# Kernel optimization log

Measured on AMD Instinct MI355X. Metric: run time of the kernel, lower is better.

The kernel has to match this reference:

```python
import jax, jax.numpy as jnp
import numpy as np

D_MODEL = 1024
NUM_HEADS = 16
HEAD_DIM = D_MODEL // NUM_HEADS


def setup_inputs() -> dict:
    key = jax.random.key(0)
    ks = jax.random.split(key, 9)
    s = 1.0 / np.sqrt(D_MODEL)
    x = jax.random.normal(ks[0], (2, 2048, D_MODEL), dtype=jnp.float32)
    Wq = jax.random.normal(ks[1], (D_MODEL, D_MODEL), dtype=jnp.float32) * s
    bq = jnp.zeros((D_MODEL,), dtype=jnp.float32)
    Wk = jax.random.normal(ks[2], (D_MODEL, D_MODEL), dtype=jnp.float32) * s
    bk = jnp.zeros((D_MODEL,), dtype=jnp.float32)
    Wv = jax.random.normal(ks[3], (D_MODEL, D_MODEL), dtype=jnp.float32) * s
    bv = jnp.zeros((D_MODEL,), dtype=jnp.float32)
    Wo = jax.random.normal(ks[4], (D_MODEL, D_MODEL), dtype=jnp.float32) * s
    bo = jnp.zeros((D_MODEL,), dtype=jnp.float32)
    return {"x": x, "Wq": Wq, "bq": bq, "Wk": Wk, "bk": bk,
            "Wv": Wv, "bv": bv, "Wo": Wo, "bo": bo}


def reference(x, Wq, bq, Wk, bk, Wv, bv, Wo, bo):
    B, S, D = x.shape
    H, Hd = NUM_HEADS, HEAD_DIM
    scale = 1.0 / np.sqrt(Hd)

    def split_heads(t):  # [B,S,D] -> [B,H,S,Hd]
        return t.reshape(B, S, H, Hd).transpose(0, 2, 1, 3)

    q = split_heads(x @ Wq + bq)
    k = split_heads(x @ Wk + bk)
    v = split_heads(x @ Wv + bv)

    scores = jnp.einsum('bhqd,bhkd->bhqk', q, k) * scale
    scores = scores - jnp.max(scores, axis=-1, keepdims=True)
    attn = jax.nn.softmax(scores, axis=-1)
    attended = jnp.einsum('bhqk,bhkd->bhqd', attn, v)
    attended = attended.transpose(0, 2, 1, 3).reshape(B, S, D)
    return attended @ Wo + bo
```

## Files before the change

kernel.cpp:

```cpp
#include <hip/hip_runtime.h>
#include <hip/hip_bf16.h>

typedef __bf16 bf16_t;
typedef __bf16 bf16x8 __attribute__((ext_vector_type(8)));
typedef __bf16 bf16x4 __attribute__((ext_vector_type(4)));
typedef float floatx4 __attribute__((ext_vector_type(4)));
typedef short short4v __attribute__((ext_vector_type(4)));

#define D_MODEL 1024
#define SEQ     2048
#define BATCH   2
#define NHEAD   16
#define HDIM    64
#define MTOT    (BATCH * SEQ)

#define QSCALE  0.18033688011112042f

union PBu { bf16x4 b; short4v s; };

__device__ __forceinline__ void async_copy16(const bf16_t* g, bf16_t* l) {
    __builtin_amdgcn_global_load_lds(
        (const __attribute__((address_space(1))) void*)g,
        (__attribute__((address_space(3))) void*)l, 16, 0, 0);
}

__global__ void cvt_f32_bf16(const float* __restrict__ x, bf16_t* __restrict__ y, int n) {
    int i = (blockIdx.x * 256 + threadIdx.x) * 4;
    if (i < n) {
        const float4 v = *(const float4*)(x + i);
        bf16x4 o = { (bf16_t)v.x, (bf16_t)v.y, (bf16_t)v.z, (bf16_t)v.w };
        *(bf16x4*)(y + i) = o;
    }
}

__global__ void transpose_w4(
    const float* __restrict__ W0, const float* __restrict__ W1,
    const float* __restrict__ W2, const float* __restrict__ W3,
    bf16_t* __restrict__ T0, bf16_t* __restrict__ T1,
    bf16_t* __restrict__ T2, bf16_t* __restrict__ T3)
{
    __shared__ float tile[32][33];
    const int z = blockIdx.z;
    const float* W = (z == 0) ? W0 : (z == 1) ? W1 : (z == 2) ? W2 : W3;
    bf16_t*     Wt = (z == 0) ? T0 : (z == 1) ? T1 : (z == 2) ? T2 : T3;
    const int tx = threadIdx.x, ty = threadIdx.y;
    const int k0 = blockIdx.y * 32, n0 = blockIdx.x * 32;
#pragma unroll
    for (int j = 0; j < 32; j += 8)
        tile[ty + j][tx] = W[(size_t)(k0 + ty + j) * D_MODEL + n0 + tx];
    __syncthreads();
#pragma unroll
    for (int j = 0; j < 32; j += 8)
        Wt[(size_t)(n0 + ty + j) * D_MODEL + k0 + tx] = (bf16_t)tile[tx][ty + j];
}

__device__ __forceinline__ void gemm_mainloop(
    const bf16_t* __restrict__ A, const bf16_t* __restrict__ Bt,
    int m0, int n0, bf16_t* As, bf16_t* Bs, floatx4 acc[4][4])
{
    const int tid  = threadIdx.x;
    const int lane = tid & 63;
    const int wid  = tid >> 6;
    const int quad = lane >> 4;
    const int col  = lane & 15;
    const int wm   = (wid >> 1) * 64;
    const int wn   = (wid & 1) * 64;
    const int srow = tid >> 3;
    const int scc  = ((tid & 7) ^ (srow & 7)) * 8;
    const int xorc = col & 7;

    const bf16_t* Ag = A  + (size_t)(m0 + srow) * D_MODEL + scc;
    const bf16_t* Bg = Bt + (size_t)(n0 + srow) * D_MODEL + scc;
    bf16_t* Al = As + tid * 8;
    bf16_t* Bl = Bs + tid * 8;

    for (int kb = 0; kb < D_MODEL; kb += 64) {
#pragma unroll
        for (int p = 0; p < 4; ++p) {
            async_copy16(Ag + kb + p * (32 * D_MODEL), Al + p * 2048);
            async_copy16(Bg + kb + p * (32 * D_MODEL), Bl + p * 2048);
        }
        __syncthreads();
#pragma unroll
        for (int kh = 0; kh < 2; ++kh) {
            bf16x8 af[4], bfr[4];
#pragma unroll
            for (int i = 0; i < 4; ++i)
                af[i] = *(const bf16x8*)(As + (wm + i * 16 + col) * 64 + (((kh * 4 + quad) ^ xorc) * 8));
#pragma unroll
            for (int j = 0; j < 4; ++j)
                bfr[j] = *(const bf16x8*)(Bs + (wn + j * 16 + col) * 64 + (((kh * 4 + quad) ^ xorc) * 8));
#pragma unroll
            for (int i = 0; i < 4; ++i)
#pragma unroll
                for (int j = 0; j < 4; ++j)
                    acc[i][j] = __builtin_amdgcn_mfma_f32_16x16x32_bf16(af[i], bfr[j], acc[i][j], 0, 0, 0);
        }
        __syncthreads();
    }
}

__global__ __launch_bounds__(256, 3) void gemm_qkv(
    const bf16_t* __restrict__ xb,
    const bf16_t* __restrict__ Wtq, const bf16_t* __restrict__ Wtk, const bf16_t* __restrict__ Wtv,
    const float* __restrict__ bq, const float* __restrict__ bk, const float* __restrict__ bv,
    bf16_t* __restrict__ Q, bf16_t* __restrict__ Kh, bf16_t* __restrict__ Vt)
{
    __shared__ bf16_t As[128 * 64];
    __shared__ bf16_t Bs[128 * 64];
    const int z = blockIdx.z;
    const bf16_t* Bt   = (z == 0) ? Wtq : (z == 1) ? Wtk : Wtv;
    const float*  bias = (z == 0) ? bq  : (z == 1) ? bk  : bv;
    bf16_t*       O    = (z == 0) ? Q   : (z == 1) ? Kh  : Vt;
    const float   qs   = (z == 0) ? QSCALE : 1.0f;
    const int m0 = blockIdx.y * 128;
    const int n0 = blockIdx.x * 128;

    floatx4 acc[4][4];
#pragma unroll
    for (int i = 0; i < 4; ++i)
#pragma unroll
        for (int j = 0; j < 4; ++j)
            acc[i][j] = (floatx4){0.f, 0.f, 0.f, 0.f};

    gemm_mainloop(xb, Bt, m0, n0, As, Bs, acc);

    const int tid  = threadIdx.x;
    const int lane = tid & 63;
    const int wid  = tid >> 6;
    const int quad = lane >> 4;
    const int col  = lane & 15;
    const int wm   = (wid >> 1) * 64;
    const int wn   = (wid & 1) * 64;

    if (z == 2) {
#pragma unroll
        for (int i = 0; i < 4; ++i) {
#pragma unroll
            for (int j = 0; j < 4; ++j) {
                const int n = n0 + wn + j * 16 + col;
                const float bb = bias[n];
                const int mb = m0 + wm + i * 16 + quad * 4;
                const size_t bhb = (size_t)((mb >> 11) * NHEAD + (n >> 6)) * (SEQ * HDIM);
                bf16x4 pk = { (bf16_t)(acc[i][j][0] + bb), (bf16_t)(acc[i][j][1] + bb),
                              (bf16_t)(acc[i][j][2] + bb), (bf16_t)(acc[i][j][3] + bb) };
                *(bf16x4*)(O + bhb + (size_t)(n & 63) * SEQ + (mb & 2047)) = pk;
            }
        }
    } else {
#pragma unroll
        for (int i = 0; i < 4; ++i) {
#pragma unroll
            for (int j = 0; j < 4; ++j) {
                const int n = n0 + wn + j * 16 + col;
                const float bb = bias[n];
#pragma unroll
                for (int r = 0; r < 4; ++r) {
                    const int m = m0 + wm + i * 16 + quad * 4 + r;
                    const float v = (acc[i][j][r] + bb) * qs;
                    const size_t bhb = (size_t)((m >> 11) * NHEAD + (n >> 6)) * (SEQ * HDIM);
                    O[bhb + (size_t)(m & 2047) * HDIM + (n & 63)] = (bf16_t)v;
                }
            }
        }
    }
}

__global__ __launch_bounds__(256, 2) void attn_kernel(
    const bf16_t* __restrict__ Q, const bf16_t* __restrict__ K,
    const bf16_t* __restrict__ Vt, bf16_t* __restrict__ A2)
{
    __shared__ union SM {
        struct { bf16_t Ks[2][64 * 64]; bf16_t Vs[2][64 * 64]; } t;
        struct { float Ored[2][64 * 68]; float Lred[2][64]; } r;
    } sm;

    const int tid  = threadIdx.x;
    const int lane = tid & 63;
    const int wid  = tid >> 6;
    const int quad = lane >> 4;
    const int col  = lane & 15;
    const int xorc = col & 7;
    const int qh   = wid & 1;
    const int kh   = wid >> 1;

    const int blk = blockIdx.x;
    const int idx = blk >> 3;
    const int bh  = (blk & 7) * 4 + (idx >> 4);
    const int q0  = (idx & 15) * 128;
    const int b   = bh >> 4, h = bh & 15;

    const bf16_t* Qb = Q  + (size_t)bh * (SEQ * HDIM);
    const bf16_t* Kb = K  + (size_t)bh * (SEQ * HDIM);
    const bf16_t* Vb = Vt + (size_t)bh * (SEQ * HDIM);

    bf16x8 qf[4][2];
#pragma unroll
    for (int g = 0; g < 4; ++g) {
        const int qrow = q0 + qh * 64 + g * 16 + col;
        qf[g][0] = *(const bf16x8*)(Qb + (size_t)qrow * HDIM + quad * 8);
        qf[g][1] = *(const bf16x8*)(Qb + (size_t)qrow * HDIM + 32 + quad * 8);
    }

    floatx4 o_acc[4][4];
    float lsum[4] = {0.f, 0.f, 0.f, 0.f};
#pragma unroll
    for (int g = 0; g < 4; ++g)
#pragma unroll
        for (int dt = 0; dt < 4; ++dt)
            o_acc[g][dt] = (floatx4){0.f, 0.f, 0.f, 0.f};

    const int srow = tid >> 3;
    const int scc  = ((tid & 7) ^ (srow & 7)) * 8;
    const bf16_t* Kg = Kb + (size_t)srow * HDIM + scc;
    const bf16_t* Vg = Vb + (size_t)srow * SEQ + scc;
    bf16_t* Ks0 = &sm.t.Ks[0][0];
    bf16_t* Ks1 = &sm.t.Ks[1][0];
    bf16_t* Vs0 = &sm.t.Vs[0][0];
    bf16_t* Vs1 = &sm.t.Vs[1][0];

    auto stage = [&](int ko, bf16_t* dk, bf16_t* dv) {
        async_copy16(Kg + (size_t)ko * HDIM, dk + tid * 8);
        async_copy16(Kg + (size_t)(ko + 32) * HDIM, dk + tid * 8 + 2048);
        async_copy16(Vg + ko, dv + tid * 8);
        async_copy16(Vg + (size_t)32 * SEQ + ko, dv + tid * 8 + 2048);
    };

    auto step = [&](const bf16_t* KsC, const bf16_t* VsC) {
        bf16x8 kf[2][2];
#pragma unroll
        for (int tt = 0; tt < 2; ++tt) {
            const int t = kh * 2 + tt;
            kf[tt][0] = *(const bf16x8*)(KsC + (t * 16 + col) * 64 + ((quad ^ xorc) * 8));
            kf[tt][1] = *(const bf16x8*)(KsC + (t * 16 + col) * 64 + (((4 + quad) ^ xorc) * 8));
        }
        short4v vfr[4][2];
#pragma unroll
        for (int dt = 0; dt < 4; ++dt)
#pragma unroll
            for (int tt = 0; tt < 2; ++tt) {
                const int t = kh * 2 + tt;
                const int sch = t * 2 + (quad >> 1);
                vfr[dt][tt] = *(const short4v*)(VsC + (dt * 16 + col) * 64 + ((sch ^ xorc) * 8) + (quad & 1) * 4);
            }
#pragma unroll
        for (int g = 0; g < 4; ++g) {
            floatx4 s_acc[2];
            short4v pb[2];
            __builtin_amdgcn_s_setprio(1);
#pragma unroll
            for (int tt = 0; tt < 2; ++tt) {
                s_acc[tt] = (floatx4){0.f, 0.f, 0.f, 0.f};
                s_acc[tt] = __builtin_amdgcn_mfma_f32_16x16x32_bf16(kf[tt][0], qf[g][0], s_acc[tt], 0, 0, 0);
                s_acc[tt] = __builtin_amdgcn_mfma_f32_16x16x32_bf16(kf[tt][1], qf[g][1], s_acc[tt], 0, 0, 0);
            }
            __builtin_amdgcn_s_setprio(0);
            float ls = 0.f;
#pragma unroll
            for (int tt = 0; tt < 2; ++tt) {
                const float p0 = __builtin_amdgcn_exp2f(s_acc[tt][0]);
                const float p1 = __builtin_amdgcn_exp2f(s_acc[tt][1]);
                const float p2 = __builtin_amdgcn_exp2f(s_acc[tt][2]);
                const float p3 = __builtin_amdgcn_exp2f(s_acc[tt][3]);
                ls += (p0 + p1) + (p2 + p3);
                PBu u;
                u.b = (bf16x4){ (bf16_t)p0, (bf16_t)p1, (bf16_t)p2, (bf16_t)p3 };
                pb[tt] = u.s;
            }
            lsum[g] += ls;
            __builtin_amdgcn_s_setprio(1);
#pragma unroll
            for (int dt = 0; dt < 4; ++dt)
#pragma unroll
                for (int tt = 0; tt < 2; ++tt)
                    o_acc[g][dt] = __builtin_amdgcn_mfma_f32_16x16x16bf16_1k(vfr[dt][tt], pb[tt], o_acc[g][dt], 0, 0, 0);
            __builtin_amdgcn_s_setprio(0);
        }
    };

    stage(0,  Ks0, Vs0);
    stage(64, Ks1, Vs1);

#pragma unroll 1
    for (int it2 = 0; it2 < 15; ++it2) {
        asm volatile("s_waitcnt vmcnt(4)" ::: "memory");
        __builtin_amdgcn_s_barrier();
        step(Ks0, Vs0);
        asm volatile("s_waitcnt lgkmcnt(0)" ::: "memory");
        __builtin_amdgcn_s_barrier();
        stage((2 * it2 + 2) * 64, Ks0, Vs0);

        asm volatile("s_waitcnt vmcnt(4)" ::: "memory");
        __builtin_amdgcn_s_barrier();
        step(Ks1, Vs1);
        asm volatile("s_waitcnt lgkmcnt(0)" ::: "memory");
        __builtin_amdgcn_s_barrier();
        stage((2 * it2 + 3) * 64, Ks1, Vs1);
    }
    asm volatile("s_waitcnt vmcnt(4)" ::: "memory");
    __builtin_amdgcn_s_barrier();
    step(Ks0, Vs0);
    asm volatile("s_waitcnt vmcnt(0)" ::: "memory");
    __builtin_amdgcn_s_barrier();
    step(Ks1, Vs1);

#pragma unroll
    for (int g = 0; g < 4; ++g) {
        lsum[g] += __shfl_xor(lsum[g], 16, 64);
        lsum[g] += __shfl_xor(lsum[g], 32, 64);
    }
    __syncthreads();
    if (kh == 1) {
#pragma unroll
        for (int g = 0; g < 4; ++g) {
#pragma unroll
            for (int dt = 0; dt < 4; ++dt)
#pragma unroll
                for (int r = 0; r < 4; ++r) {
                    const int d = dt * 16 + quad * 4 + r;
                    sm.r.Ored[qh][d * 68 + g * 16 + col] = o_acc[g][dt][r];
                }
            if (quad == 0)
                sm.r.Lred[qh][g * 16 + col] = lsum[g];
        }
    }
    __syncthreads();
    if (kh == 0) {
#pragma unroll
        for (int g = 0; g < 4; ++g) {
            const float l = lsum[g] + sm.r.Lred[qh][g * 16 + col];
            const float inv = 1.0f / l;
            const int qrow = q0 + qh * 64 + g * 16 + col;
            bf16_t* dst = A2 + ((size_t)(b * SEQ + qrow)) * D_MODEL + h * HDIM + quad * 4;
#pragma unroll
            for (int dt = 0; dt < 4; ++dt) {
                bf16x4 pk;
#pragma unroll
                for (int r = 0; r < 4; ++r) {
                    const int d = dt * 16 + quad * 4 + r;
                    pk[r] = (bf16_t)((o_acc[g][dt][r] + sm.r.Ored[qh][d * 68 + g * 16 + col]) * inv);
                }
                *(bf16x4*)(dst + dt * 16) = pk;
            }
        }
    }
}

__global__ __launch_bounds__(256, 3) void gemm_proj(
    const bf16_t* __restrict__ A2, const bf16_t* __restrict__ Wto,
    const float* __restrict__ bo, float* __restrict__ out)
{
    __shared__ bf16_t As[64 * 64];
    __shared__ bf16_t Bs[128 * 64];
    const int m0 = blockIdx.y * 64;
    const int n0 = blockIdx.x * 128;

    const int tid  = threadIdx.x;
    const int lane = tid & 63;
    const int wid  = tid >> 6;
    const int quad = lane >> 4;
    const int col  = lane & 15;
    const int wm   = (wid >> 1) * 32;
    const int wn   = (wid & 1) * 64;
    const int srow = tid >> 3;
    const int scc  = ((tid & 7) ^ (srow & 7)) * 8;
    const int xorc = col & 7;

    floatx4 acc[2][4];
#pragma unroll
    for (int i = 0; i < 2; ++i)
#pragma unroll
        for (int j = 0; j < 4; ++j)
            acc[i][j] = (floatx4){0.f, 0.f, 0.f, 0.f};

    const bf16_t* Ag = A2  + (size_t)(m0 + srow) * D_MODEL + scc;
    const bf16_t* Bg = Wto + (size_t)(n0 + srow) * D_MODEL + scc;
    bf16_t* Al = As + tid * 8;
    bf16_t* Bl = Bs + tid * 8;

    for (int kb = 0; kb < D_MODEL; kb += 64) {
#pragma unroll
        for (int p = 0; p < 2; ++p)
            async_copy16(Ag + kb + p * (32 * D_MODEL), Al + p * 2048);
#pragma unroll
        for (int p = 0; p < 4; ++p)
            async_copy16(Bg + kb + p * (32 * D_MODEL), Bl + p * 2048);
        __syncthreads();
#pragma unroll
        for (int kh = 0; kh < 2; ++kh) {
            bf16x8 af[2], bfr[4];
#pragma unroll
            for (int i = 0; i < 2; ++i)
                af[i] = *(const bf16x8*)(As + (wm + i * 16 + col) * 64 + (((kh * 4 + quad) ^ xorc) * 8));
#pragma unroll
            for (int j = 0; j < 4; ++j)
                bfr[j] = *(const bf16x8*)(Bs + (wn + j * 16 + col) * 64 + (((kh * 4 + quad) ^ xorc) * 8));
#pragma unroll
            for (int i = 0; i < 2; ++i)
#pragma unroll
                for (int j = 0; j < 4; ++j)
                    acc[i][j] = __builtin_amdgcn_mfma_f32_16x16x32_bf16(af[i], bfr[j], acc[i][j], 0, 0, 0);
        }
        __syncthreads();
    }

#pragma unroll
    for (int i = 0; i < 2; ++i) {
#pragma unroll
        for (int j = 0; j < 4; ++j) {
            const int n = n0 + wn + j * 16 + col;
            const float bb = bo[n];
#pragma unroll
            for (int r = 0; r < 4; ++r) {
                const int m = m0 + wm + i * 16 + quad * 4 + r;
                out[(size_t)m * D_MODEL + n] = acc[i][j][r] + bb;
            }
        }
    }
}

extern "C" void kernel_launch(void* const* d_in, const int* in_sizes, int n_in,
                              void* d_out, int out_size, void* d_ws, size_t ws_size,
                              hipStream_t stream) {
    const float* x  = (const float*)d_in[0];
    const float* Wq = (const float*)d_in[1];
    const float* bq = (const float*)d_in[2];
    const float* Wk = (const float*)d_in[3];
    const float* bk = (const float*)d_in[4];
    const float* Wv = (const float*)d_in[5];
    const float* bv = (const float*)d_in[6];
    const float* Wo = (const float*)d_in[7];
    const float* bo = (const float*)d_in[8];
    float* out = (float*)d_out;

    const size_t MB = 1ull << 20;
    char* ws = (char*)d_ws;
    bf16_t* Q     = (bf16_t*)(ws + 0 * MB);
    bf16_t* Kh    = (bf16_t*)(ws + 8 * MB);
    bf16_t* Vt    = (bf16_t*)(ws + 16 * MB);
    bf16_t* A2    = (bf16_t*)(ws + 24 * MB);
    bf16_t* xb    = (bf16_t*)(ws + 32 * MB);
    bf16_t* Wtq   = (bf16_t*)(ws + 40 * MB);
    bf16_t* Wtk   = (bf16_t*)(ws + 42 * MB);
    bf16_t* Wtv   = (bf16_t*)(ws + 44 * MB);
    bf16_t* Wto   = (bf16_t*)(ws + 46 * MB);

    const int nx = MTOT * D_MODEL;
    cvt_f32_bf16<<<nx / (256 * 4), 256, 0, stream>>>(x, xb, nx);

    transpose_w4<<<dim3(D_MODEL / 32, D_MODEL / 32, 4), dim3(32, 8), 0, stream>>>(
        Wq, Wk, Wv, Wo, Wtq, Wtk, Wtv, Wto);

    gemm_qkv<<<dim3(D_MODEL / 128, MTOT / 128, 3), 256, 0, stream>>>(
        xb, Wtq, Wtk, Wtv, bq, bk, bv, Q, Kh, Vt);

    attn_kernel<<<dim3(512), 256, 0, stream>>>(Q, Kh, Vt, A2);

    gemm_proj<<<dim3(D_MODEL / 128, MTOT / 64), 256, 0, stream>>>(A2, Wto, bo, out);
}
```

Measured before the change: 188.9 us.

## Software-pipeline PV MFMAs one tile behind QK and merge prep kernels

The attention inner loop now computes the QK scores and exponentials for the current K/V tile while issuing the P·V MFMAs for the previous tile. V fragments and P values are double-buffered in registers so exp/convert work can overlap matrix-core work. Separately, the x-to-bf16 conversion is folded into the weight-transpose kernel as an extra grid slice, which removes one launch. The added register buffers raise register pressure and may reduce occupancy.

```diff
diff --git a/kernel.cpp b/kernel.cpp
--- a/kernel.cpp
+++ b/kernel.cpp
@@ -24,16 +24,8 @@
         (__attribute__((address_space(3))) void*)l, 16, 0, 0);
 }
 
-__global__ void cvt_f32_bf16(const float* __restrict__ x, bf16_t* __restrict__ y, int n) {
-    int i = (blockIdx.x * 256 + threadIdx.x) * 4;
-    if (i < n) {
-        const float4 v = *(const float4*)(x + i);
-        bf16x4 o = { (bf16_t)v.x, (bf16_t)v.y, (bf16_t)v.z, (bf16_t)v.w };
-        *(bf16x4*)(y + i) = o;
-    }
-}
-
-__global__ void transpose_w4(
+__global__ void prep(
+    const float* __restrict__ x, bf16_t* __restrict__ xb,
     const float* __restrict__ W0, const float* __restrict__ W1,
     const float* __restrict__ W2, const float* __restrict__ W3,
     bf16_t* __restrict__ T0, bf16_t* __restrict__ T1,
@@ -41,9 +33,21 @@
 {
     __shared__ float tile[32][33];
     const int z = blockIdx.z;
+    const int tx = threadIdx.x, ty = threadIdx.y;
+    if (z == 4) {
+        const int tid = ty * 32 + tx;
+        const int base = (blockIdx.y * 32 + blockIdx.x) * 4096 + tid * 4;
+#pragma unroll
+        for (int r = 0; r < 4; ++r) {
+            const int i = base + r * 1024;
+            const float4 v = *(const float4*)(x + i);
+            bf16x4 o = { (bf16_t)v.x, (bf16_t)v.y, (bf16_t)v.z, (bf16_t)v.w };
+            *(bf16x4*)(xb + i) = o;
+        }
+        return;
+    }
     const float* W = (z == 0) ? W0 : (z == 1) ? W1 : (z == 2) ? W2 : W3;
     bf16_t*     Wt = (z == 0) ? T0 : (z == 1) ? T1 : (z == 2) ? T2 : T3;
-    const int tx = threadIdx.x, ty = threadIdx.y;
     const int k0 = blockIdx.y * 32, n0 = blockIdx.x * 32;
 #pragma unroll
     for (int j = 0; j < 32; j += 8)
@@ -226,7 +230,26 @@
         async_copy16(Vg + (size_t)32 * SEQ + ko, dv + tid * 8 + 2048);
     };
 
-    auto step = [&](const bf16_t* KsC, const bf16_t* VsC) {
+    short4v vfrA[4][2], vfrB[4][2];
+    short4v pbA[4][2],  pbB[4][2];
+
+    auto pv = [&](short4v (&vfrP)[4][2], short4v (&pbP)[4][2]) {
+        __builtin_amdgcn_s_setprio(1);
+#pragma unroll
+        for (int g = 0; g < 4; ++g)
+#pragma unroll
+            for (int dt = 0; dt < 4; ++dt)
+#pragma unroll
+                for (int tt = 0; tt < 2; ++tt)
+                    o_acc[g][dt] = __builtin_amdgcn_mfma_f32_16x16x16bf16_1k(
+                        vfrP[dt][tt], pbP[g][tt], o_acc[g][dt], 0, 0, 0);
+        __builtin_amdgcn_s_setprio(0);
+    };
+
+    auto tilestep = [&](const bf16_t* KsC, const bf16_t* VsC,
+                        short4v (&vfrC)[4][2], short4v (&pbC)[4][2],
+                        short4v (&vfrP)[4][2], short4v (&pbP)[4][2],
+                        bool doPV) {
         bf16x8 kf[2][2];
 #pragma unroll
         for (int tt = 0; tt < 2; ++tt) {
@@ -234,19 +257,18 @@
             kf[tt][0] = *(const bf16x8*)(KsC + (t * 16 + col) * 64 + ((quad ^ xorc) * 8));
             kf[tt][1] = *(const bf16x8*)(KsC + (t * 16 + col) * 64 + (((4 + quad) ^ xorc) * 8));
         }
-        short4v vfr[4][2];
 #pragma unroll
         for (int dt = 0; dt < 4; ++dt)
 #pragma unroll
             for (int tt = 0; tt < 2; ++tt) {
                 const int t = kh * 2 + tt;
                 const int sch = t * 2 + (quad >> 1);
-                vfr[dt][tt] = *(const short4v*)(VsC + (dt * 16 + col) * 64 + ((sch ^ xorc) * 8) + (quad & 1) * 4);
-            }
+                vfrC[dt][tt] = *(const short4v*)(VsC + (dt * 16 + col) * 64 + ((sch ^ xorc) * 8) + (quad & 1) * 4);
+            }
+        if (doPV) pv(vfrP, pbP);
 #pragma unroll
         for (int g = 0; g < 4; ++g) {
             floatx4 s_acc[2];
-            short4v pb[2];
             __builtin_amdgcn_s_setprio(1);
 #pragma unroll
             for (int tt = 0; tt < 2; ++tt) {
@@ -265,44 +287,42 @@
                 ls += (p0 + p1) + (p2 + p3);
                 PBu u;
                 u.b = (bf16x4){ (bf16_t)p0, (bf16_t)p1, (bf16_t)p2, (bf16_t)p3 };
-                pb[tt] = u.s;
+                pbC[g][tt] = u.s;
             }
             lsum[g] += ls;
-            __builtin_amdgcn_s_setprio(1);
-#pragma unroll
-            for (int dt = 0; dt < 4; ++dt)
-#pragma unroll
-                for (int tt = 0; tt < 2; ++tt)
-                    o_acc[g][dt] = __builtin_amdgcn_mfma_f32_16x16x16bf16_1k(vfr[dt][tt], pb[tt], o_acc[g][dt], 0, 0, 0);
-            __builtin_amdgcn_s_setprio(0);
         }
     };
 
     stage(0,  Ks0, Vs0);
     stage(64, Ks1, Vs1);
 
+    asm volatile("s_waitcnt vmcnt(4)" ::: "memory");
+    __builtin_amdgcn_s_barrier();
+    tilestep(Ks0, Vs0, vfrA, pbA, vfrB, pbB, false);
+    asm volatile("s_waitcnt lgkmcnt(0)" ::: "memory");
+    __builtin_amdgcn_s_barrier();
+    stage(2 * 64, Ks0, Vs0);
+
 #pragma unroll 1
-    for (int it2 = 0; it2 < 15; ++it2) {
+    for (int p = 0; p < 15; ++p) {
         asm volatile("s_waitcnt vmcnt(4)" ::: "memory");
         __builtin_amdgcn_s_barrier();
-        step(Ks0, Vs0);
+        tilestep(Ks1, Vs1, vfrB, pbB, vfrA, pbA, true);
         asm volatile("s_waitcnt lgkmcnt(0)" ::: "memory");
         __builtin_amdgcn_s_barrier();
-        stage((2 * it2 + 2) * 64, Ks0, Vs0);
+        stage((2 * p + 3) * 64, Ks1, Vs1);
 
         asm volatile("s_waitcnt vmcnt(4)" ::: "memory");
         __builtin_amdgcn_s_barrier();
-        step(Ks1, Vs1);
+        tilestep(Ks0, Vs0, vfrA, pbA, vfrB, pbB, true);
         asm volatile("s_waitcnt lgkmcnt(0)" ::: "memory");
         __builtin_amdgcn_s_barrier();
-        stage((2 * it2 + 3) * 64, Ks1, Vs1);
-    }
-    asm volatile("s_waitcnt vmcnt(4)" ::: "memory");
-    __builtin_amdgcn_s_barrier();
-    step(Ks0, Vs0);
+        if (p < 14) stage((2 * p + 4) * 64, Ks0, Vs0);
+    }
     asm volatile("s_waitcnt vmcnt(0)" ::: "memory");
     __builtin_amdgcn_s_barrier();
-    step(Ks1, Vs1);
+    tilestep(Ks1, Vs1, vfrB, pbB, vfrA, pbA, true);
+    pv(vfrB, pbB);
 
 #pragma unroll
     for (int g = 0; g < 4; ++g) {
@@ -445,11 +465,8 @@
     bf16_t* Wtv   = (bf16_t*)(ws + 44 * MB);
     bf16_t* Wto   = (bf16_t*)(ws + 46 * MB);
 
-    const int nx = MTOT * D_MODEL;
-    cvt_f32_bf16<<<nx / (256 * 4), 256, 0, stream>>>(x, xb, nx);
-
-    transpose_w4<<<dim3(D_MODEL / 32, D_MODEL / 32, 4), dim3(32, 8), 0, stream>>>(
-        Wq, Wk, Wv, Wo, Wtq, Wtk, Wtv, Wto);
+    prep<<<dim3(32, 32, 5), dim3(32, 8), 0, stream>>>(
+        x, xb, Wq, Wk, Wv, Wo, Wtq, Wtk, Wtv, Wto);
 
     gemm_qkv<<<dim3(D_MODEL / 128, MTOT / 128, 3), 256, 0, stream>>>(
         xb, Wtq, Wtk, Wtv, bq, bk, bv, Q, Kh, Vt);
```

After: 181.3 us, median of 4. 1.04x faster.
